# Kernel tuning notes

Hardware: AMD Instinct MI355X
Metric: run time of the kernel (lower is better)

Reference implementation:

```python
import jax, jax.numpy as jnp
import numpy as np

B, N_IN, D = 2, 262144, 32
N_OUT, K, NK = 65536, 4, 9
MIN_DIST = 0.01


def setup_inputs() -> dict:
    key = jax.random.key(0)
    k1, k2, k3, k4 = jax.random.split(key, 4)
    x_level_in = jax.random.normal(k1, (B, N_IN, D), dtype=jnp.float32)
    coords_in = jax.random.uniform(k2, (2, B, N_IN), dtype=jnp.float32)
    coords_out = jax.random.uniform(k3, (2, B, N_OUT, K), dtype=jnp.float32)
    neighbor_idx = jax.random.randint(k4, (B, N_OUT, K, NK), 0, N_IN)
    sigma = jnp.ones((D,), dtype=jnp.float32) * (MIN_DIST * 200.0)
    return {
        "x_level_in": x_level_in,
        "coords_in": coords_in,
        "coords_out": coords_out,
        "sigma": sigma,
        "neighbor_idx": neighbor_idx,
    }


def reference(x_level_in, coords_in, coords_out, sigma, neighbor_idx):
    # x_level_in: [B, N_in, D]; coords_in: [2, B, N_in]
    # coords_out: [2, B, N_out, K]; neighbor_idx: [B, N_out, K, NK]; sigma: [D]
    b = jnp.arange(x_level_in.shape[0])[:, None, None, None]  # batch index broadcaster
    # gather neighbor coordinates across the input grid: [2, B, N_out, K, NK]
    nb_coords = coords_in[:, b, neighbor_idx]
    # squared euclidean distance in (lon, lat): [B, N_out, K, NK]
    d2 = jnp.sum((coords_out[..., None] - nb_coords) ** 2, axis=0)
    # per-channel Gaussian/RBF weights: [B, N_out, K, NK, D]
    w = jnp.exp(-d2[..., None] / (2.0 * sigma ** 2))
    # gather neighbor features: [B, N_out, K, NK, D]
    feats = x_level_in[b, neighbor_idx]
    # normalized weighted aggregate over the NK neighbors: [B, N_out, K, D]
    num = jnp.sum(w * feats, axis=3)
    den = jnp.sum(w, axis=3) + 1e-9
    x = num / den
    # flatten (N_out, K) -> sequence dim, as in forward's final view
    return x.reshape(x.shape[0], -1, x.shape[-1])
```

## Files before the change

### kernel.cpp

```cpp
#include <hip/hip_runtime.h>
#include <hip/hip_fp16.h>

constexpr int B        = 2;
constexpr int N_IN     = 262144;
constexpr int D        = 32;
constexpr int N_OUT    = 65536;
constexpr int K        = 4;
constexpr int NK       = 9;
constexpr int P        = B * N_OUT * K;
constexpr int PPB      = N_OUT * K;
constexpr size_t XTOT  = (size_t)B * N_IN * D;
constexpr int NPH      = 4;

typedef _Float16 half2v __attribute__((ext_vector_type(2)));
typedef _Float16 half8v __attribute__((ext_vector_type(8)));
typedef float    f4v    __attribute__((ext_vector_type(4)));

template<int L>
__device__ __forceinline__ int qbcast_i(int v) {
    return __builtin_amdgcn_mov_dpp(v, L * 0x55, 0xf, 0xf, true);
}
template<int L>
__device__ __forceinline__ float qbcast_f(float v) {
    return __int_as_float(
        __builtin_amdgcn_mov_dpp(__float_as_int(v), L * 0x55, 0xf, 0xf, true));
}

__global__ __launch_bounds__(256) void prep_kernel(
    const float* __restrict__ x,   _Float16* __restrict__ xh,
    const float* __restrict__ cin, half2v*   __restrict__ cp)
{
    const int tid  = blockIdx.x * 256 + threadIdx.x;
    const size_t i = (size_t)tid * 8;
    const f4v a = __builtin_nontemporal_load(reinterpret_cast<const f4v*>(x + i));
    const f4v b = __builtin_nontemporal_load(reinterpret_cast<const f4v*>(x + i) + 1);
    half8v h;
    h[0] = (_Float16)a[0]; h[1] = (_Float16)a[1];
    h[2] = (_Float16)a[2]; h[3] = (_Float16)a[3];
    h[4] = (_Float16)b[0]; h[5] = (_Float16)b[1];
    h[6] = (_Float16)b[2]; h[7] = (_Float16)b[3];
    *reinterpret_cast<half8v*>(xh + i) = h;
    if (tid < B * N_IN) {
        half2v c;
        c[0] = (_Float16)cin[tid];
        c[1] = (_Float16)cin[B * N_IN + tid];
        cp[tid] = c;
    }
}

__global__ __launch_bounds__(256) void projection_kernel_h(
    const _Float16* __restrict__ xh,
    const half2v*   __restrict__ cpack,
    const float*    __restrict__ coords_out,
    const float*    __restrict__ sigma,
    const int*      __restrict__ nidx,
    float*          __restrict__ out)
{
    const int bid   = blockIdx.x;
    const int xcd   = bid & 7;
    const int j     = bid >> 3;
    const int batch = xcd >> 2;
    const int bbi   = j * 4 + (xcd & 3);
    const int point = batch * PPB + bbi * 64 + (threadIdx.x >> 2);
    const int h     = threadIdx.x & 3;

    const int cbase = batch * N_IN;

    const float cox = __builtin_nontemporal_load(coords_out + point);
    const float coy = __builtin_nontemporal_load(coords_out + P + point);

    const float4 sg0 = *reinterpret_cast<const float4*>(sigma + h * 8);
    const float4 sg1 = *reinterpret_cast<const float4*>(sigma + h * 8 + 4);
    float s[8];
    s[0] = 1.0f / (2.0f * sg0.x * sg0.x); s[1] = 1.0f / (2.0f * sg0.y * sg0.y);
    s[2] = 1.0f / (2.0f * sg0.z * sg0.z); s[3] = 1.0f / (2.0f * sg0.w * sg0.w);
    s[4] = 1.0f / (2.0f * sg1.x * sg1.x); s[5] = 1.0f / (2.0f * sg1.y * sg1.y);
    s[6] = 1.0f / (2.0f * sg1.z * sg1.z); s[7] = 1.0f / (2.0f * sg1.w * sg1.w);
    bool uni = true;
    #pragma unroll
    for (int k = 1; k < 8; ++k) uni = uni && (s[k] == s[0]);

    const int* __restrict__ ip = nidx + (size_t)point * NK;
    const int ia = __builtin_nontemporal_load(ip + h);
    const int ib = __builtin_nontemporal_load(ip + 4 + h);
    const int i8 = __builtin_nontemporal_load(ip + 8);

    const half2v ca = cpack[cbase + ia];
    const half2v cb = cpack[cbase + ib];
    const half2v c8 = cpack[cbase + i8];

    int idxs[NK];
    idxs[0] = qbcast_i<0>(ia); idxs[1] = qbcast_i<1>(ia);
    idxs[2] = qbcast_i<2>(ia); idxs[3] = qbcast_i<3>(ia);
    idxs[4] = qbcast_i<0>(ib); idxs[5] = qbcast_i<1>(ib);
    idxs[6] = qbcast_i<2>(ib); idxs[7] = qbcast_i<3>(ib);
    idxs[8] = i8;

    const float dxa = cox - (float)ca[0], dya = coy - (float)ca[1];
    const float dxb = cox - (float)cb[0], dyb = coy - (float)cb[1];
    const float dx8 = cox - (float)c8[0], dy8 = coy - (float)c8[1];
    const float d2a = dxa * dxa + dya * dya;
    const float d2b = dxb * dxb + dyb * dyb;
    const float d28 = dx8 * dx8 + dy8 * dy8;

    float num[8];
    #pragma unroll
    for (int k = 0; k < 8; ++k) num[k] = 0.f;

    if (uni) {
        const float wa = __expf(-d2a * s[0]);
        const float wb = __expf(-d2b * s[0]);
        const float w8 = __expf(-d28 * s[0]);
        float w[NK];
        w[0] = qbcast_f<0>(wa); w[1] = qbcast_f<1>(wa);
        w[2] = qbcast_f<2>(wa); w[3] = qbcast_f<3>(wa);
        w[4] = qbcast_f<0>(wb); w[5] = qbcast_f<1>(wb);
        w[6] = qbcast_f<2>(wb); w[7] = qbcast_f<3>(wb);
        w[8] = w8;
        float den = 0.f;
        #pragma unroll
        for (int t = 0; t < NK; ++t) den += w[t];

        for (int ph = 0; ph < NPH; ++ph) {
            #pragma unroll
            for (int t = 0; t < NK; ++t) {
                if ((idxs[t] >> 16) == ph) {
                    const half8v f = *reinterpret_cast<const half8v*>(
                        xh + (size_t)(cbase + idxs[t]) * D + h * 8);
                    #pragma unroll
                    for (int k = 0; k < 8; ++k) num[k] += w[t] * (float)f[k];
                }
            }
            if (ph != NPH - 1) __syncthreads();
        }

        float* op = out + (size_t)point * D + h * 8;
        const float r = 1.0f / (den + 1e-9f);
        f4v o0, o1;
        o0[0] = num[0] * r; o0[1] = num[1] * r;
        o0[2] = num[2] * r; o0[3] = num[3] * r;
        o1[0] = num[4] * r; o1[1] = num[5] * r;
        o1[2] = num[6] * r; o1[3] = num[7] * r;
        __builtin_nontemporal_store(o0, reinterpret_cast<f4v*>(op));
        __builtin_nontemporal_store(o1, reinterpret_cast<f4v*>(op + 4));
    } else {
        float den[8];
        #pragma unroll
        for (int k = 0; k < 8; ++k) den[k] = 0.f;
        float d2v[NK];
        d2v[0] = qbcast_f<0>(d2a); d2v[1] = qbcast_f<1>(d2a);
        d2v[2] = qbcast_f<2>(d2a); d2v[3] = qbcast_f<3>(d2a);
        d2v[4] = qbcast_f<0>(d2b); d2v[5] = qbcast_f<1>(d2b);
        d2v[6] = qbcast_f<2>(d2b); d2v[7] = qbcast_f<3>(d2b);
        d2v[8] = d28;
        #pragma unroll
        for (int t = 0; t < NK; ++t) {
            const half8v f = *reinterpret_cast<const half8v*>(
                xh + (size_t)(cbase + idxs[t]) * D + h * 8);
            #pragma unroll
            for (int k = 0; k < 8; ++k) {
                const float wk = __expf(-d2v[t] * s[k]);
                num[k] += wk * (float)f[k];
                den[k] += wk;
            }
        }
        float* op = out + (size_t)point * D + h * 8;
        f4v o0, o1;
        o0[0] = num[0] / (den[0] + 1e-9f); o0[1] = num[1] / (den[1] + 1e-9f);
        o0[2] = num[2] / (den[2] + 1e-9f); o0[3] = num[3] / (den[3] + 1e-9f);
        o1[0] = num[4] / (den[4] + 1e-9f); o1[1] = num[5] / (den[5] + 1e-9f);
        o1[2] = num[6] / (den[6] + 1e-9f); o1[3] = num[7] / (den[7] + 1e-9f);
        __builtin_nontemporal_store(o0, reinterpret_cast<f4v*>(op));
        __builtin_nontemporal_store(o1, reinterpret_cast<f4v*>(op + 4));
    }
}

__global__ __launch_bounds__(256) void projection_kernel_f32(
    const float* __restrict__ x,
    const float* __restrict__ coords_in,
    const float* __restrict__ coords_out,
    const float* __restrict__ sigma,
    const int*   __restrict__ nidx,
    float*       __restrict__ out)
{
    const int tid   = blockIdx.x * 256 + threadIdx.x;
    const int point = tid >> 3;
    const int q     = tid & 7;
    const int b     = point / PPB;
    const int cbase = b * N_IN;

    const float cox = coords_out[point];
    const float coy = coords_out[P + point];

    const float4 sg = *reinterpret_cast<const float4*>(sigma + q * 4);
    const float s0 = 1.0f / (2.0f * sg.x * sg.x);
    const float s1 = 1.0f / (2.0f * sg.y * sg.y);
    const float s2 = 1.0f / (2.0f * sg.z * sg.z);
    const float s3 = 1.0f / (2.0f * sg.w * sg.w);

    float4 num = make_float4(0.f, 0.f, 0.f, 0.f);
    float4 den = make_float4(0.f, 0.f, 0.f, 0.f);
    const int* __restrict__ ip = nidx + (size_t)point * NK;

    #pragma unroll
    for (int nk = 0; nk < NK; ++nk) {
        const int idx = ip[nk];
        const float cx = coords_in[cbase + idx];
        const float cy = coords_in[B * N_IN + cbase + idx];
        const float dx = cox - cx;
        const float dy = coy - cy;
        const float d2 = dx * dx + dy * dy;
        const float4 f = *reinterpret_cast<const float4*>(
            x + (size_t)(cbase + idx) * D + q * 4);
        const float w0 = __expf(-d2 * s0);
        const float w1 = __expf(-d2 * s1);
        const float w2 = __expf(-d2 * s2);
        const float w3 = __expf(-d2 * s3);
        num.x += w0 * f.x;  den.x += w0;
        num.y += w1 * f.y;  den.y += w1;
        num.z += w2 * f.z;  den.z += w2;
        num.w += w3 * f.w;  den.w += w3;
    }

    float4 o;
    o.x = num.x / (den.x + 1e-9f);
    o.y = num.y / (den.y + 1e-9f);
    o.z = num.z / (den.z + 1e-9f);
    o.w = num.w / (den.w + 1e-9f);
    *reinterpret_cast<float4*>(out + (size_t)point * D + q * 4) = o;
}

extern "C" void kernel_launch(void* const* d_in, const int* in_sizes, int n_in,
                              void* d_out, int out_size, void* d_ws, size_t ws_size,
                              hipStream_t stream) {
    const float* x      = (const float*)d_in[0];
    const float* cin    = (const float*)d_in[1];
    const float* cout_  = (const float*)d_in[2];
    const float* sigma  = (const float*)d_in[3];
    const int*   nidx   = (const int*)  d_in[4];
    float*       outp   = (float*)d_out;

    const int block = 256;

    const size_t xh_bytes = XTOT * sizeof(_Float16);
    const size_t cp_bytes = (size_t)B * N_IN * sizeof(half2v);

    if (ws_size >= xh_bytes + cp_bytes) {
        _Float16* xh = (_Float16*)d_ws;
        half2v*   cp = (half2v*)((char*)d_ws + xh_bytes);
        prep_kernel<<<(int)(XTOT / 8 / block), block, 0, stream>>>(x, xh, cin, cp);
        const int grid_main = (P * 4) / block;
        projection_kernel_h<<<grid_main, block, 0, stream>>>(
            xh, cp, cout_, sigma, nidx, outp);
    } else {
        const int grid_main = (P * 8) / block;
        projection_kernel_f32<<<grid_main, block, 0, stream>>>(
            x, cin, cout_, sigma, nidx, outp);
    }
}
```

Baseline: 259.7 us.

## Convert projection to persistent grid with grid-wide barrier between iterations

The projection kernel now launches a fixed grid of 1024 blocks, each processing 8 chunks of 64 points in sequence. Between chunks all blocks meet at a bounded-spin global atomic barrier so the grid advances through the index-phase ordering in lockstep, aiming for better cache locality on the gathers. The non-uniform-sigma path moves to a scalar slow_point fallback run by one lane per point. The barrier adds atomic and spin overhead and assumes all 1024 blocks are resident at once; the spin cap bounds the wait if they are not.

```diff
diff --git a/kernel.cpp b/kernel.cpp
--- a/kernel.cpp
+++ b/kernel.cpp
@@ -10,7 +10,9 @@
 constexpr int P        = B * N_OUT * K;
 constexpr int PPB      = N_OUT * K;
 constexpr size_t XTOT  = (size_t)B * N_IN * D;
-constexpr int NPH      = 4;
+constexpr int NPH       = 4;
+constexpr int GRID_MAIN = 1024;
+constexpr int ITERS     = 8;
 
 typedef _Float16 half2v __attribute__((ext_vector_type(2)));
 typedef _Float16 half8v __attribute__((ext_vector_type(8)));
@@ -28,7 +30,8 @@
 
 __global__ __launch_bounds__(256) void prep_kernel(
     const float* __restrict__ x,   _Float16* __restrict__ xh,
-    const float* __restrict__ cin, half2v*   __restrict__ cp)
+    const float* __restrict__ cin, half2v*   __restrict__ cp,
+    unsigned int* __restrict__ bar)
 {
     const int tid  = blockIdx.x * 256 + threadIdx.x;
     const size_t i = (size_t)tid * 8;
@@ -46,28 +49,68 @@
         c[1] = (_Float16)cin[B * N_IN + tid];
         cp[tid] = c;
     }
-}
-
-__global__ __launch_bounds__(256) void projection_kernel_h(
+    if (blockIdx.x == 0 && threadIdx.x < ITERS)
+        __hip_atomic_store(bar + threadIdx.x, 0u,
+                           __ATOMIC_RELAXED, __HIP_MEMORY_SCOPE_AGENT);
+}
+
+__device__ void slow_point(
+    int p, int cbase, const _Float16* __restrict__ xb,
+    const half2v* __restrict__ cpack, const float* __restrict__ coords_out,
+    const float* __restrict__ sigma, const int* __restrict__ nidx,
+    float* __restrict__ out)
+{
+    const float cox = coords_out[p];
+    const float coy = coords_out[P + p];
+    const int* __restrict__ ip = nidx + (size_t)p * NK;
+    int id[NK]; float d2[NK];
+    #pragma unroll
+    for (int t = 0; t < NK; ++t) id[t] = ip[t];
+    #pragma unroll
+    for (int t = 0; t < NK; ++t) {
+        const half2v c = cpack[cbase + id[t]];
+        const float dx = cox - (float)c[0], dy = coy - (float)c[1];
+        d2[t] = dx * dx + dy * dy;
+    }
+    for (int q = 0; q < 4; ++q) {
+        float n[8], d[8], s[8];
+        #pragma unroll
+        for (int k = 0; k < 8; ++k) {
+            n[k] = 0.f; d[k] = 0.f;
+            const float g = sigma[q * 8 + k];
+            s[k] = 1.0f / (2.0f * g * g);
+        }
+        #pragma unroll
+        for (int t = 0; t < NK; ++t) {
+            const half8v f = *reinterpret_cast<const half8v*>(xb + id[t] * D + q * 8);
+            #pragma unroll
+            for (int k = 0; k < 8; ++k) {
+                const float w = __expf(-d2[t] * s[k]);
+                n[k] += w * (float)f[k];
+                d[k] += w;
+            }
+        }
+        #pragma unroll
+        for (int k = 0; k < 8; ++k)
+            out[(size_t)p * D + q * 8 + k] = n[k] / (d[k] + 1e-9f);
+    }
+}
+
+__global__ __launch_bounds__(256) void projection_conv_kernel(
     const _Float16* __restrict__ xh,
     const half2v*   __restrict__ cpack,
     const float*    __restrict__ coords_out,
     const float*    __restrict__ sigma,
     const int*      __restrict__ nidx,
-    float*          __restrict__ out)
+    float*          __restrict__ out,
+    unsigned int*   __restrict__ bar)
 {
     const int bid   = blockIdx.x;
     const int xcd   = bid & 7;
-    const int j     = bid >> 3;
     const int batch = xcd >> 2;
-    const int bbi   = j * 4 + (xcd & 3);
-    const int point = batch * PPB + bbi * 64 + (threadIdx.x >> 2);
+    const int wbase = (bid >> 3) * 4 + (xcd & 3);
     const int h     = threadIdx.x & 3;
-
     const int cbase = batch * N_IN;
-
-    const float cox = __builtin_nontemporal_load(coords_out + point);
-    const float coy = __builtin_nontemporal_load(coords_out + P + point);
 
     const float4 sg0 = *reinterpret_cast<const float4*>(sigma + h * 8);
     const float4 sg1 = *reinterpret_cast<const float4*>(sigma + h * 8 + 4);
@@ -79,38 +122,54 @@
     bool uni = true;
     #pragma unroll
     for (int k = 1; k < 8; ++k) uni = uni && (s[k] == s[0]);
-
-    const int* __restrict__ ip = nidx + (size_t)point * NK;
-    const int ia = __builtin_nontemporal_load(ip + h);
-    const int ib = __builtin_nontemporal_load(ip + 4 + h);
-    const int i8 = __builtin_nontemporal_load(ip + 8);
-
-    const half2v ca = cpack[cbase + ia];
-    const half2v cb = cpack[cbase + ib];
-    const half2v c8 = cpack[cbase + i8];
-
-    int idxs[NK];
-    idxs[0] = qbcast_i<0>(ia); idxs[1] = qbcast_i<1>(ia);
-    idxs[2] = qbcast_i<2>(ia); idxs[3] = qbcast_i<3>(ia);
-    idxs[4] = qbcast_i<0>(ib); idxs[5] = qbcast_i<1>(ib);
-    idxs[6] = qbcast_i<2>(ib); idxs[7] = qbcast_i<3>(ib);
-    idxs[8] = i8;
-
-    const float dxa = cox - (float)ca[0], dya = coy - (float)ca[1];
-    const float dxb = cox - (float)cb[0], dyb = coy - (float)cb[1];
-    const float dx8 = cox - (float)c8[0], dy8 = coy - (float)c8[1];
-    const float d2a = dxa * dxa + dya * dya;
-    const float d2b = dxb * dxb + dyb * dyb;
-    const float d28 = dx8 * dx8 + dy8 * dy8;
-
-    float num[8];
-    #pragma unroll
-    for (int k = 0; k < 8; ++k) num[k] = 0.f;
-
-    if (uni) {
-        const float wa = __expf(-d2a * s[0]);
-        const float wb = __expf(-d2b * s[0]);
-        const float w8 = __expf(-d28 * s[0]);
+    {
+        const float g0 = sigma[0];
+        const float ss = 1.0f / (2.0f * g0 * g0);
+        uni = uni && (s[0] == ss);
+    }
+
+    if (!uni) {
+        if (h == 0) {
+            for (int jj = 0; jj < ITERS; ++jj) {
+                const int p = batch * PPB + wbase * 512 + jj * 64 +
+                              (threadIdx.x >> 2);
+                slow_point(p, cbase, xh + (size_t)cbase * D, cpack,
+                           coords_out, sigma, nidx, out);
+            }
+        }
+        return;
+    }
+    const float s0 = s[0];
+
+    for (int jj = 0; jj < ITERS; ++jj) {
+        const int point = batch * PPB + wbase * 512 + jj * 64 + (threadIdx.x >> 2);
+
+        const float cox = __builtin_nontemporal_load(coords_out + point);
+        const float coy = __builtin_nontemporal_load(coords_out + P + point);
+
+        const int* __restrict__ ip = nidx + (size_t)point * NK;
+        const int ia = __builtin_nontemporal_load(ip + h);
+        const int ib = __builtin_nontemporal_load(ip + 4 + h);
+        const int i8 = __builtin_nontemporal_load(ip + 8);
+
+        const half2v ca = cpack[cbase + ia];
+        const half2v cb = cpack[cbase + ib];
+        const half2v c8 = cpack[cbase + i8];
+
+        int idxs[NK];
+        idxs[0] = qbcast_i<0>(ia); idxs[1] = qbcast_i<1>(ia);
+        idxs[2] = qbcast_i<2>(ia); idxs[3] = qbcast_i<3>(ia);
+        idxs[4] = qbcast_i<0>(ib); idxs[5] = qbcast_i<1>(ib);
+        idxs[6] = qbcast_i<2>(ib); idxs[7] = qbcast_i<3>(ib);
+        idxs[8] = i8;
+
+        const float dxa = cox - (float)ca[0], dya = coy - (float)ca[1];
+        const float dxb = cox - (float)cb[0], dyb = coy - (float)cb[1];
+        const float dx8 = cox - (float)c8[0], dy8 = coy - (float)c8[1];
+
+        const float wa = __expf(-(dxa * dxa + dya * dya) * s0);
+        const float wb = __expf(-(dxb * dxb + dyb * dyb) * s0);
+        const float w8 = __expf(-(dx8 * dx8 + dy8 * dy8) * s0);
         float w[NK];
         w[0] = qbcast_f<0>(wa); w[1] = qbcast_f<1>(wa);
         w[2] = qbcast_f<2>(wa); w[3] = qbcast_f<3>(wa);
@@ -120,6 +179,10 @@
         float den = 0.f;
         #pragma unroll
         for (int t = 0; t < NK; ++t) den += w[t];
+
+        float num[8];
+        #pragma unroll
+        for (int k = 0; k < 8; ++k) num[k] = 0.f;
 
         for (int ph = 0; ph < NPH; ++ph) {
             #pragma unroll
@@ -143,35 +206,22 @@
         o1[2] = num[6] * r; o1[3] = num[7] * r;
         __builtin_nontemporal_store(o0, reinterpret_cast<f4v*>(op));
         __builtin_nontemporal_store(o1, reinterpret_cast<f4v*>(op + 4));
-    } else {
-        float den[8];
-        #pragma unroll
-        for (int k = 0; k < 8; ++k) den[k] = 0.f;
-        float d2v[NK];
-        d2v[0] = qbcast_f<0>(d2a); d2v[1] = qbcast_f<1>(d2a);
-        d2v[2] = qbcast_f<2>(d2a); d2v[3] = qbcast_f<3>(d2a);
-        d2v[4] = qbcast_f<0>(d2b); d2v[5] = qbcast_f<1>(d2b);
-        d2v[6] = qbcast_f<2>(d2b); d2v[7] = qbcast_f<3>(d2b);
-        d2v[8] = d28;
-        #pragma unroll
-        for (int t = 0; t < NK; ++t) {
-            const half8v f = *reinterpret_cast<const half8v*>(
-                xh + (size_t)(cbase + idxs[t]) * D + h * 8);
-            #pragma unroll
-            for (int k = 0; k < 8; ++k) {
-                const float wk = __expf(-d2v[t] * s[k]);
-                num[k] += wk * (float)f[k];
-                den[k] += wk;
+
+        if (jj != ITERS - 1) {
+            __syncthreads();
+            if (threadIdx.x == 0) {
+                __hip_atomic_fetch_add(bar + jj, 1u,
+                                       __ATOMIC_RELAXED, __HIP_MEMORY_SCOPE_AGENT);
+                int spins = 0;
+                while (__hip_atomic_load(bar + jj, __ATOMIC_RELAXED,
+                                         __HIP_MEMORY_SCOPE_AGENT)
+                           < (unsigned)GRID_MAIN && spins < 512) {
+                    __builtin_amdgcn_s_sleep(2);
+                    ++spins;
+                }
             }
-        }
-        float* op = out + (size_t)point * D + h * 8;
-        f4v o0, o1;
-        o0[0] = num[0] / (den[0] + 1e-9f); o0[1] = num[1] / (den[1] + 1e-9f);
-        o0[2] = num[2] / (den[2] + 1e-9f); o0[3] = num[3] / (den[3] + 1e-9f);
-        o1[0] = num[4] / (den[4] + 1e-9f); o1[1] = num[5] / (den[5] + 1e-9f);
-        o1[2] = num[6] / (den[6] + 1e-9f); o1[3] = num[7] / (den[7] + 1e-9f);
-        __builtin_nontemporal_store(o0, reinterpret_cast<f4v*>(op));
-        __builtin_nontemporal_store(o1, reinterpret_cast<f4v*>(op + 4));
+            __syncthreads();
+        }
     }
 }
 
@@ -245,13 +295,14 @@
     const size_t xh_bytes = XTOT * sizeof(_Float16);
     const size_t cp_bytes = (size_t)B * N_IN * sizeof(half2v);
 
-    if (ws_size >= xh_bytes + cp_bytes) {
-        _Float16* xh = (_Float16*)d_ws;
-        half2v*   cp = (half2v*)((char*)d_ws + xh_bytes);
-        prep_kernel<<<(int)(XTOT / 8 / block), block, 0, stream>>>(x, xh, cin, cp);
-        const int grid_main = (P * 4) / block;
-        projection_kernel_h<<<grid_main, block, 0, stream>>>(
-            xh, cp, cout_, sigma, nidx, outp);
+    if (ws_size >= xh_bytes + cp_bytes + 64) {
+        _Float16*     xh  = (_Float16*)d_ws;
+        half2v*       cp  = (half2v*)((char*)d_ws + xh_bytes);
+        unsigned int* bar = (unsigned int*)((char*)d_ws + xh_bytes + cp_bytes);
+        prep_kernel<<<(int)(XTOT / 8 / block), block, 0, stream>>>(
+            x, xh, cin, cp, bar);
+        projection_conv_kernel<<<GRID_MAIN, block, 0, stream>>>(
+            xh, cp, cout_, sigma, nidx, outp, bar);
     } else {
         const int grid_main = (P * 8) / block;
         projection_kernel_f32<<<grid_main, block, 0, stream>>>(
```

Result: slower. 804.2 us (+209.7%).

## Remove phased barrier gather; issue all neighbor feature loads up front

Applied to the files above, without the earlier changes.

Drops the four-phase loop that split neighbor gathers by index range with __syncthreads between phases, which was meant to localize cache traffic. All nine half8 feature loads are now issued before the weight computation so their latencies overlap, and the output epilogue is shared by both branches. This gives up the phased cache-locality scheme, raises register pressure from holding nine vectors, and replaces the multiply by a reciprocal with per-lane division.

```diff
diff --git a/kernel.cpp b/kernel.cpp
--- a/kernel.cpp
+++ b/kernel.cpp
@@ -10,7 +10,6 @@
 constexpr int P        = B * N_OUT * K;
 constexpr int PPB      = N_OUT * K;
 constexpr size_t XTOT  = (size_t)B * N_IN * D;
-constexpr int NPH      = 4;
 
 typedef _Float16 half2v __attribute__((ext_vector_type(2)));
 typedef _Float16 half8v __attribute__((ext_vector_type(8)));
@@ -96,6 +95,12 @@
     idxs[6] = qbcast_i<2>(ib); idxs[7] = qbcast_i<3>(ib);
     idxs[8] = i8;
 
+    half8v f[NK];
+    #pragma unroll
+    for (int t = 0; t < NK; ++t)
+        f[t] = *reinterpret_cast<const half8v*>(
+            xh + (size_t)(cbase + idxs[t]) * D + h * 8);
+
     const float dxa = cox - (float)ca[0], dya = coy - (float)ca[1];
     const float dxb = cox - (float)cb[0], dyb = coy - (float)cb[1];
     const float dx8 = cox - (float)c8[0], dy8 = coy - (float)c8[1];
@@ -106,6 +111,9 @@
     float num[8];
     #pragma unroll
     for (int k = 0; k < 8; ++k) num[k] = 0.f;
+    float den[8];
+    #pragma unroll
+    for (int k = 0; k < 8; ++k) den[k] = 0.f;
 
     if (uni) {
         const float wa = __expf(-d2a * s[0]);
@@ -117,36 +125,16 @@
         w[4] = qbcast_f<0>(wb); w[5] = qbcast_f<1>(wb);
         w[6] = qbcast_f<2>(wb); w[7] = qbcast_f<3>(wb);
         w[8] = w8;
-        float den = 0.f;
+        float d0 = 0.f;
         #pragma unroll
-        for (int t = 0; t < NK; ++t) den += w[t];
-
-        for (int ph = 0; ph < NPH; ++ph) {
+        for (int t = 0; t < NK; ++t) {
+            d0 += w[t];
             #pragma unroll
-            for (int t = 0; t < NK; ++t) {
-                if ((idxs[t] >> 16) == ph) {
-                    const half8v f = *reinterpret_cast<const half8v*>(
-                        xh + (size_t)(cbase + idxs[t]) * D + h * 8);
-                    #pragma unroll
-                    for (int k = 0; k < 8; ++k) num[k] += w[t] * (float)f[k];
-                }
-            }
-            if (ph != NPH - 1) __syncthreads();
+            for (int k = 0; k < 8; ++k) num[k] += w[t] * (float)f[t][k];
         }
-
-        float* op = out + (size_t)point * D + h * 8;
-        const float r = 1.0f / (den + 1e-9f);
-        f4v o0, o1;
-        o0[0] = num[0] * r; o0[1] = num[1] * r;
-        o0[2] = num[2] * r; o0[3] = num[3] * r;
-        o1[0] = num[4] * r; o1[1] = num[5] * r;
-        o1[2] = num[6] * r; o1[3] = num[7] * r;
-        __builtin_nontemporal_store(o0, reinterpret_cast<f4v*>(op));
-        __builtin_nontemporal_store(o1, reinterpret_cast<f4v*>(op + 4));
+        #pragma unroll
+        for (int k = 0; k < 8; ++k) den[k] = d0;
     } else {
-        float den[8];
-        #pragma unroll
-        for (int k = 0; k < 8; ++k) den[k] = 0.f;
         float d2v[NK];
         d2v[0] = qbcast_f<0>(d2a); d2v[1] = qbcast_f<1>(d2a);
         d2v[2] = qbcast_f<2>(d2a); d2v[3] = qbcast_f<3>(d2a);
@@ -155,24 +143,23 @@
         d2v[8] = d28;
         #pragma unroll
         for (int t = 0; t < NK; ++t) {
-            const half8v f = *reinterpret_cast<const half8v*>(
-                xh + (size_t)(cbase + idxs[t]) * D + h * 8);
             #pragma unroll
             for (int k = 0; k < 8; ++k) {
                 const float wk = __expf(-d2v[t] * s[k]);
-                num[k] += wk * (float)f[k];
+                num[k] += wk * (float)f[t][k];
                 den[k] += wk;
             }
         }
-        float* op = out + (size_t)point * D + h * 8;
-        f4v o0, o1;
-        o0[0] = num[0] / (den[0] + 1e-9f); o0[1] = num[1] / (den[1] + 1e-9f);
-        o0[2] = num[2] / (den[2] + 1e-9f); o0[3] = num[3] / (den[3] + 1e-9f);
-        o1[0] = num[4] / (den[4] + 1e-9f); o1[1] = num[5] / (den[5] + 1e-9f);
-        o1[2] = num[6] / (den[6] + 1e-9f); o1[3] = num[7] / (den[7] + 1e-9f);
-        __builtin_nontemporal_store(o0, reinterpret_cast<f4v*>(op));
-        __builtin_nontemporal_store(o1, reinterpret_cast<f4v*>(op + 4));
-    }
+    }
+
+    float* op = out + (size_t)point * D + h * 8;
+    f4v o0, o1;
+    o0[0] = num[0] / (den[0] + 1e-9f); o0[1] = num[1] / (den[1] + 1e-9f);
+    o0[2] = num[2] / (den[2] + 1e-9f); o0[3] = num[3] / (den[3] + 1e-9f);
+    o1[0] = num[4] / (den[4] + 1e-9f); o1[1] = num[5] / (den[5] + 1e-9f);
+    o1[2] = num[6] / (den[6] + 1e-9f); o1[3] = num[7] / (den[7] + 1e-9f);
+    __builtin_nontemporal_store(o0, reinterpret_cast<f4v*>(op));
+    __builtin_nontemporal_store(o1, reinterpret_cast<f4v*>(op + 4));
 }
 
 __global__ __launch_bounds__(256) void projection_kernel_f32(
```

Result: faster. 215.7 us (-16.9%).
